# Kernel optimization log

Measured on AMD Instinct MI355X. Metric: run time of the kernel, lower is better.

Reference implementation:

```python
import jax, jax.numpy as jnp
import numpy as np

NUM_SIN = 8
HIDDEN = 64
COND = 128
OUT = 4
SQRT2 = 1.4142135623730951


def coords_to_sinusoidals(coords):
    # coords: [..., 2]; per-frequency blocks of 4: [sin_x, sin_y, cos_x, cos_y]
    freqs = 2.0 ** jnp.arange(NUM_SIN, dtype=coords.dtype)  # mult freq_type, multiplier=2
    ang = coords[..., None, :] * freqs[:, None]              # [..., 8, 2]
    emb = jnp.concatenate([jnp.sin(ang), jnp.cos(ang)], axis=-1)  # [..., 8, 4]
    return emb.reshape(coords.shape[:-1] + (2 * 2 * NUM_SIN,))


def equal_linear(x, w, b, lrelu):
    scale = 1.0 / np.sqrt(w.shape[1])  # lr_mul = 1
    y = x @ (w * scale).T + b
    if lrelu:
        y = jax.nn.leaky_relu(y, 0.2) * SQRT2  # fused_lrelu
    return y


def setup_inputs() -> dict:
    key = jax.random.key(0)
    ks = jax.random.split(key, 8)
    coords = jax.random.normal(ks[0], (8, 256, 256, 2), dtype=jnp.float32)
    c = jax.random.normal(ks[1], (8, COND), dtype=jnp.float32)
    freq_unlock = jax.random.uniform(ks[2], (1,), dtype=jnp.float32)
    in1 = 2 * 2 * NUM_SIN + COND  # 160
    in2 = HIDDEN + COND           # 192
    w1 = jax.random.normal(ks[3], (HIDDEN, in1), dtype=jnp.float32)
    w2 = jax.random.normal(ks[4], (HIDDEN, in2), dtype=jnp.float32)
    w3 = jax.random.normal(ks[5], (HIDDEN, in2), dtype=jnp.float32)
    w4 = jax.random.normal(ks[6], (OUT, in2), dtype=jnp.float32)
    b1 = jnp.zeros((HIDDEN,), jnp.float32)
    b2 = jnp.zeros((HIDDEN,), jnp.float32)
    b3 = jnp.zeros((HIDDEN,), jnp.float32)
    b4 = jnp.zeros((OUT,), jnp.float32)
    return {"coords": coords, "c": c, "freq_unlock": freq_unlock,
            "w1": w1, "b1": b1, "w2": w2, "b2": b2,
            "w3": w3, "b3": b3, "w4": w4, "b4": b4}


def reference(coords, c, freq_unlock, w1, b1, w2, b2, w3, b3, w4, b4):
    B, H, W, _ = coords.shape
    emb = coords_to_sinusoidals(coords / 10.0)  # [B,H,W,32]
    # progressive frequency masking
    limits = jnp.arange(1, NUM_SIN + 1, dtype=coords.dtype) / (NUM_SIN + 1)
    weights = jnp.clip((freq_unlock[0] - limits) * (NUM_SIN + 1), 0.0, 1.0)  # [8]
    emb = emb * jnp.repeat(weights, 4)  # blocks of 4 per frequency
    x = emb.reshape(B * H * W, -1)
    cf = jnp.broadcast_to(c[:, None, None, :], (B, H, W, COND)).reshape(B * H * W, COND)
    h = equal_linear(jnp.concatenate([x, cf], -1), w1, b1, True)
    h = equal_linear(jnp.concatenate([h, cf], -1), w2, b2, True)
    h = equal_linear(jnp.concatenate([h, cf], -1), w3, b3, True)
    h = equal_linear(jnp.concatenate([h, cf], -1), w4, b4, False)
    out = h.reshape(B, H, W, OUT)
    # radius masking
    radius = jnp.sqrt(jnp.sum(coords ** 2, axis=-1, keepdims=True))
    out = out * (1.0 - jnp.tanh(jax.nn.relu(radius - 1.0)))
    return out
```

## Files before the change

kernel.cpp:

```cpp
#include <hip/hip_runtime.h>
#include <math.h>


typedef _Float16 half2v __attribute__((ext_vector_type(2)));
typedef __fp16   fp16x2 __attribute__((ext_vector_type(2)));
typedef _Float16 half4v __attribute__((ext_vector_type(4)));
typedef _Float16 half8  __attribute__((ext_vector_type(8)));
typedef float f32x16 __attribute__((ext_vector_type(16)));

#define SCALE1 0.0790569415042094833f
#define SCALE2 0.0721687836487032206f
#define SQRT2F 1.41421356237309515f

#define FE_L1 0
#define FE_L2 256
#define FE_L3 768
#define FE_L4 1280
#define FE_TOT 1536
#define OFF_CB1 6144
#define OFF_CB2 6656
#define OFF_CB3 7168
#define OFF_CB4 7680

__global__ __launch_bounds__(256) void prep_kernel(
    const float* __restrict__ c, const float* __restrict__ fu,
    const float* __restrict__ w1, const float* __restrict__ b1,
    const float* __restrict__ w2, const float* __restrict__ b2,
    const float* __restrict__ w3, const float* __restrict__ b3,
    const float* __restrict__ w4, const float* __restrict__ b4,
    float* __restrict__ ws)
{
  int t = blockIdx.x * 256 + threadIdx.x;
  if (t < 12288) {
    _Float16* fr = (_Float16*)ws;
    int e, Ktm;
    const float* w; float scale; int stride; bool perm;
    if (t < 2048)       { e = t;         Ktm = 2; w = w1; scale = SCALE1;          stride = 160; perm = false; }
    else if (t < 6144)  { e = t - 2048;  Ktm = 4; w = w2; scale = SCALE2 * SQRT2F; stride = 192; perm = true;  }
    else if (t < 10240) { e = t - 6144;  Ktm = 4; w = w3; scale = SCALE2 * SQRT2F; stride = 192; perm = true;  }
    else                { e = t - 10240; Ktm = 4; w = w4; scale = SCALE2 * SQRT2F; stride = 192; perm = true;  }
    int til  = e >> 9;
    int lane = (e >> 3) & 63;
    int r    = e & 7;
    int q    = lane >> 5;
    int mt = til / Ktm, kt = til - mt * Ktm;
    int j = 32 * mt + (lane & 31);
    int k;
    if (perm) {
      k = 32 * (kt >> 1) + 16 * (kt & 1) + 8 * (r >> 2) + 4 * q + (r & 3);
    } else {
      k = 16 * kt + 8 * q + r;
    }
    float val;
    if (t < 2048) {
      float mw = (fu[0] - (float)((k >> 2) + 1) * (1.0f / 9.0f)) * 9.0f;
      mw = fminf(fmaxf(mw, 0.0f), 1.0f);
      val = w[j * stride + k] * scale * mw;
    } else if (t >= 10240) {
      val = (j < 4) ? w[j * stride + k] * scale : 0.0f;
    } else {
      val = w[j * stride + k] * scale;
    }
    fr[t] = (_Float16)val;
  } else if (t < 12288 + 2048) {
    int u = t - 12288;
    int grp = u >> 9;
    const float* wr; float bias; float scale; int outoff;
    int b, j;
    if (grp < 3) {
      b = (u & 511) >> 6; j = u & 63;
      if (grp == 0)      { wr = w1 + j * 160 + 32; bias = b1[j]; scale = SCALE1; outoff = OFF_CB1 + b * 64 + j; }
      else if (grp == 1) { wr = w2 + j * 192 + 64; bias = b2[j]; scale = SCALE2; outoff = OFF_CB2 + b * 64 + j; }
      else               { wr = w3 + j * 192 + 64; bias = b3[j]; scale = SCALE2; outoff = OFF_CB3 + b * 64 + j; }
    } else {
      int u2 = u - 1536;
      if (u2 >= 32) return;
      b = u2 >> 2; j = u2 & 3;
      wr = w4 + j * 192 + 64; bias = b4[j]; scale = SCALE2; outoff = OFF_CB4 + b * 4 + j;
    }
    const float4* wv = (const float4*)wr;
    const float4* cv = (const float4*)(c + b * 128);
    float4 s = make_float4(0.f, 0.f, 0.f, 0.f);
    #pragma unroll
    for (int k = 0; k < 32; ++k) {
      float4 a = wv[k], d = cv[k];
      s.x = fmaf(a.x, d.x, s.x);
      s.y = fmaf(a.y, d.y, s.y);
      s.z = fmaf(a.z, d.z, s.z);
      s.w = fmaf(a.w, d.w, s.w);
    }
    float dot = (s.x + s.y) + (s.z + s.w);
    ws[outoff] = fmaf(scale, dot, bias);
  }
}

__global__ __launch_bounds__(256, 4) void decoder_main(
    const float2* __restrict__ coords, const float* __restrict__ ws,
    float4* __restrict__ out)
{
  __shared__ __align__(16) _Float16 sfr_raw[FE_TOT * 8];
  __shared__ __align__(16) float scb[256];
  half8* __restrict__ sfr = (half8*)sfr_raw;

  const int tid  = threadIdx.x;
  const int lane = tid & 63;
  const int wave = tid >> 6;
  const int b    = blockIdx.x >> 7;
  const int col  = lane & 31;
  const bool hi  = lane >= 32;
  const int q4   = hi ? 4 : 0;

  const half8* __restrict__ gfr = (const half8*)ws;
  #pragma unroll
  for (int i = 0; i < 6; ++i) {
    const int e0 = wave * 64 + 256 * i;
    __builtin_amdgcn_global_load_lds(
        (const __attribute__((address_space(1))) void*)(gfr + e0 + lane),
        (__attribute__((address_space(3))) void*)(sfr_raw + e0 * 8),
        16, 0, 0);
  }
  if (wave == 3) {
    __builtin_amdgcn_global_load_lds(
        (const __attribute__((address_space(1))) void*)(ws + OFF_CB1 + b * 64 + lane),
        (__attribute__((address_space(3))) void*)(scb + 0), 4, 0, 0);
    __builtin_amdgcn_global_load_lds(
        (const __attribute__((address_space(1))) void*)(ws + OFF_CB2 + b * 64 + lane),
        (__attribute__((address_space(3))) void*)(scb + 64), 4, 0, 0);
    __builtin_amdgcn_global_load_lds(
        (const __attribute__((address_space(1))) void*)(ws + OFF_CB3 + b * 64 + lane),
        (__attribute__((address_space(3))) void*)(scb + 128), 4, 0, 0);
    __builtin_amdgcn_global_load_lds(
        (const __attribute__((address_space(1))) void*)(ws + OFF_CB4 + b * 4 + lane),
        (__attribute__((address_space(3))) void*)(scb + 192), 4, 0, 0);
  }

  const float2* __restrict__ cptr = coords + blockIdx.x * 512 + wave * 64;
  float2 cc[2][2];
  cc[0][0] = cptr[col];       cc[0][1] = cptr[32 + col];
  cc[1][0] = cptr[256 + col]; cc[1][1] = cptr[288 + col];

  f32x16 acc[2][2];
  half8 nbf[2][4];

  auto transition = [&]() {
    #pragma unroll
    for (int mt = 0; mt < 2; ++mt)
      #pragma unroll
      for (int nt = 0; nt < 2; ++nt) {
        #pragma unroll
        for (int h = 0; h < 2; ++h) {
          half2v pp[4];
          #pragma unroll
          for (int p = 0; p < 4; ++p) {
            fp16x2 t = __builtin_amdgcn_cvt_pkrtz(acc[mt][nt][8 * h + 2 * p],
                                                  acc[mt][nt][8 * h + 2 * p + 1]);
            pp[p] = __builtin_bit_cast(half2v, t);
          }
          half4v q0 = __builtin_shufflevector(pp[0], pp[1], 0, 1, 2, 3);
          half4v q1 = __builtin_shufflevector(pp[2], pp[3], 0, 1, 2, 3);
          half8 f = __builtin_shufflevector(q0, q1, 0, 1, 2, 3, 4, 5, 6, 7);
          half8 f2 = f * (_Float16)0.2f;
          nbf[nt][2 * mt + h] = __builtin_elementwise_max(f, f2);
        }
      }
  };

  auto init_acc = [&](const float* __restrict__ cb) {
    #pragma unroll
    for (int mt = 0; mt < 2; ++mt)
      #pragma unroll
      for (int g = 0; g < 4; ++g) {
        const float4 f = *(const float4*)(cb + 32 * mt + 8 * g + q4);
        #pragma unroll
        for (int nt = 0; nt < 2; ++nt) {
          acc[mt][nt][4 * g + 0] = f.x;
          acc[mt][nt][4 * g + 1] = f.y;
          acc[mt][nt][4 * g + 2] = f.z;
          acc[mt][nt][4 * g + 3] = f.w;
        }
      }
  };

  #pragma unroll
  for (int t = 0; t < 2; ++t) {
    half8 bf[2][2];
    {
      const float qm = hi ? 0.4f : 0.1f;
      auto chain = [](float a, float* s, float* c) {
        float s0 = __sinf(a), c0 = __cosf(a);
        s[0] = s0; c[0] = c0;
        float s1 = 2.f * s0 * c0, c1 = (c0 - s0) * (c0 + s0);
        s[1] = s1; c[1] = c1;
        float s2 = 2.f * s1 * c1, c2 = (c1 - s1) * (c1 + s1);
        float s3 = 2.f * s2 * c2, c3 = (c2 - s2) * (c2 + s2);
        float s4 = 2.f * s3 * c3, c4 = (c3 - s3) * (c3 + s3);
        s[2] = s4; c[2] = c4;
        float s5 = 2.f * s4 * c4, c5 = (c4 - s4) * (c4 + s4);
        s[3] = s5; c[3] = c5;
      };
      #pragma unroll
      for (int nt = 0; nt < 2; ++nt) {
        const float2 ccv = cc[t][nt];
        float sx[4], cx[4], sy[4], cy[4];
        chain(ccv.x * qm, sx, cx);
        chain(ccv.y * qm, sy, cy);
        #pragma unroll
        for (int kt = 0; kt < 2; ++kt) {
          const int i0 = 2 * kt, i1 = 2 * kt + 1;
          half2v p0v = __builtin_bit_cast(half2v, __builtin_amdgcn_cvt_pkrtz(sx[i0], sy[i0]));
          half2v p1v = __builtin_bit_cast(half2v, __builtin_amdgcn_cvt_pkrtz(cx[i0], cy[i0]));
          half2v p2v = __builtin_bit_cast(half2v, __builtin_amdgcn_cvt_pkrtz(sx[i1], sy[i1]));
          half2v p3v = __builtin_bit_cast(half2v, __builtin_amdgcn_cvt_pkrtz(cx[i1], cy[i1]));
          half4v q0 = __builtin_shufflevector(p0v, p1v, 0, 1, 2, 3);
          half4v q1 = __builtin_shufflevector(p2v, p3v, 0, 1, 2, 3);
          bf[nt][kt] = __builtin_shufflevector(q0, q1, 0, 1, 2, 3, 4, 5, 6, 7);
        }
      }
    }

    if (t == 0) __syncthreads();

    init_acc(scb + 0);
    #pragma unroll
    for (int kt = 0; kt < 2; ++kt) {
      half8 a0 = sfr[FE_L1 + (0 * 2 + kt) * 64 + lane];
      half8 a1 = sfr[FE_L1 + (1 * 2 + kt) * 64 + lane];
      acc[0][0] = __builtin_amdgcn_mfma_f32_32x32x16_f16(a0, bf[0][kt], acc[0][0], 0, 0, 0);
      acc[0][1] = __builtin_amdgcn_mfma_f32_32x32x16_f16(a0, bf[1][kt], acc[0][1], 0, 0, 0);
      acc[1][0] = __builtin_amdgcn_mfma_f32_32x32x16_f16(a1, bf[0][kt], acc[1][0], 0, 0, 0);
      acc[1][1] = __builtin_amdgcn_mfma_f32_32x32x16_f16(a1, bf[1][kt], acc[1][1], 0, 0, 0);
    }
    transition();

    #pragma unroll
    for (int layer = 0; layer < 2; ++layer) {
      const int fe = layer == 0 ? FE_L2 : FE_L3;
      init_acc(layer == 0 ? scb + 64 : scb + 128);
      #pragma unroll
      for (int kt = 0; kt < 4; ++kt) {
        half8 a0 = sfr[fe + (0 * 4 + kt) * 64 + lane];
        half8 a1 = sfr[fe + (1 * 4 + kt) * 64 + lane];
        acc[0][0] = __builtin_amdgcn_mfma_f32_32x32x16_f16(a0, nbf[0][kt], acc[0][0], 0, 0, 0);
        acc[0][1] = __builtin_amdgcn_mfma_f32_32x32x16_f16(a0, nbf[1][kt], acc[0][1], 0, 0, 0);
        acc[1][0] = __builtin_amdgcn_mfma_f32_32x32x16_f16(a1, nbf[0][kt], acc[1][0], 0, 0, 0);
        acc[1][1] = __builtin_amdgcn_mfma_f32_32x32x16_f16(a1, nbf[1][kt], acc[1][1], 0, 0, 0);
      }
      transition();
    }

    f32x16 acc4[2];
    {
      const float c0 = scb[192], c1 = scb[193], c2 = scb[194], c3 = scb[195];
      #pragma unroll
      for (int r = 0; r < 16; ++r) { acc4[0][r] = 0.f; acc4[1][r] = 0.f; }
      if (!hi) {
        acc4[0][0] = c0; acc4[0][1] = c1; acc4[0][2] = c2; acc4[0][3] = c3;
        acc4[1][0] = c0; acc4[1][1] = c1; acc4[1][2] = c2; acc4[1][3] = c3;
      }
    }
    #pragma unroll
    for (int kt = 0; kt < 4; ++kt) {
      half8 a0 = sfr[FE_L4 + kt * 64 + lane];
      acc4[0] = __builtin_amdgcn_mfma_f32_32x32x16_f16(a0, nbf[0][kt], acc4[0], 0, 0, 0);
      acc4[1] = __builtin_amdgcn_mfma_f32_32x32x16_f16(a0, nbf[1][kt], acc4[1], 0, 0, 0);
    }

    if (!hi) {
      const int pbase = blockIdx.x * 512 + t * 256 + wave * 64 + col;
      #pragma unroll
      for (int nt = 0; nt < 2; ++nt) {
        const float2 ccv = cc[t][nt];
        const float rad = sqrtf(ccv.x * ccv.x + ccv.y * ccv.y);
        const float tt = fmaxf(rad - 1.0f, 0.0f);
        const float m = 2.0f / (__expf(2.0f * tt) + 1.0f);
        out[pbase + 32 * nt] = make_float4(acc4[nt][0] * m, acc4[nt][1] * m,
                                           acc4[nt][2] * m, acc4[nt][3] * m);
      }
    }
  }
}

extern "C" void kernel_launch(void* const* d_in, const int* in_sizes, int n_in,
                              void* d_out, int out_size, void* d_ws, size_t ws_size,
                              hipStream_t stream) {
  const float* coords = (const float*)d_in[0];
  const float* c      = (const float*)d_in[1];
  const float* fu     = (const float*)d_in[2];
  const float* w1     = (const float*)d_in[3];
  const float* b1     = (const float*)d_in[4];
  const float* w2     = (const float*)d_in[5];
  const float* b2     = (const float*)d_in[6];
  const float* w3     = (const float*)d_in[7];
  const float* b3     = (const float*)d_in[8];
  const float* w4     = (const float*)d_in[9];
  const float* b4     = (const float*)d_in[10];
  float* ws  = (float*)d_ws;
  float* out = (float*)d_out;

  int npix = in_sizes[0] / 2;

  prep_kernel<<<56, 256, 0, stream>>>(c, fu, w1, b1, w2, b2, w3, b3, w4, b4, ws);
  decoder_main<<<npix / 512, 256, 0, stream>>>(
      (const float2*)coords, ws, (float4*)out);
}
```

Before: 95.67 us.

## Split weight staging waits per layer and parallelize prep dot products

The decoder kernel now issues coordinate loads first, then bias and weight LDS loads in two halves. It replaces the single __syncthreads with partial vmcnt waits plus s_barrier, so layers 1-2 can start while layer 3-4 weights are still arriving. The prep kernel splits each 128-wide conditioning dot product across four lanes with shuffle reductions and launches more blocks to shorten its critical path. The hand-written waitcnt counts rely on the compiler's load ordering, which the sched_barrier calls are meant to preserve.

```diff
diff --git a/kernel.cpp b/kernel.cpp
--- a/kernel.cpp
+++ b/kernel.cpp
@@ -62,37 +62,43 @@
       val = w[j * stride + k] * scale;
     }
     fr[t] = (_Float16)val;
-  } else if (t < 12288 + 2048) {
+  } else {
     int u = t - 12288;
-    int grp = u >> 9;
+    if (u >= 6272) return;
+    int d = u >> 2, part = u & 3;
     const float* wr; float bias; float scale; int outoff;
     int b, j;
-    if (grp < 3) {
-      b = (u & 511) >> 6; j = u & 63;
+    if (d < 1536) {
+      int grp = d >> 9;
+      b = (d & 511) >> 6; j = d & 63;
       if (grp == 0)      { wr = w1 + j * 160 + 32; bias = b1[j]; scale = SCALE1; outoff = OFF_CB1 + b * 64 + j; }
       else if (grp == 1) { wr = w2 + j * 192 + 64; bias = b2[j]; scale = SCALE2; outoff = OFF_CB2 + b * 64 + j; }
       else               { wr = w3 + j * 192 + 64; bias = b3[j]; scale = SCALE2; outoff = OFF_CB3 + b * 64 + j; }
     } else {
-      int u2 = u - 1536;
-      if (u2 >= 32) return;
+      int u2 = d - 1536;
       b = u2 >> 2; j = u2 & 3;
       wr = w4 + j * 192 + 64; bias = b4[j]; scale = SCALE2; outoff = OFF_CB4 + b * 4 + j;
     }
-    const float4* wv = (const float4*)wr;
-    const float4* cv = (const float4*)(c + b * 128);
+    const float4* wv = (const float4*)wr + part * 8;
+    const float4* cv = (const float4*)(c + b * 128) + part * 8;
     float4 s = make_float4(0.f, 0.f, 0.f, 0.f);
     #pragma unroll
-    for (int k = 0; k < 32; ++k) {
-      float4 a = wv[k], d = cv[k];
-      s.x = fmaf(a.x, d.x, s.x);
-      s.y = fmaf(a.y, d.y, s.y);
-      s.z = fmaf(a.z, d.z, s.z);
-      s.w = fmaf(a.w, d.w, s.w);
-    }
-    float dot = (s.x + s.y) + (s.z + s.w);
-    ws[outoff] = fmaf(scale, dot, bias);
+    for (int k = 0; k < 8; ++k) {
+      float4 a = wv[k], dd = cv[k];
+      s.x = fmaf(a.x, dd.x, s.x);
+      s.y = fmaf(a.y, dd.y, s.y);
+      s.z = fmaf(a.z, dd.z, s.z);
+      s.w = fmaf(a.w, dd.w, s.w);
+    }
+    float v = (s.x + s.y) + (s.z + s.w);
+    v += __shfl_xor(v, 1);
+    v += __shfl_xor(v, 2);
+    if (part == 0) ws[outoff] = fmaf(scale, v, bias);
   }
 }
+
+#define WAIT_VM3() asm volatile("s_waitcnt vmcnt(3)" ::: "memory")
+#define WAIT_VM0() asm volatile("s_waitcnt vmcnt(0)" ::: "memory")
 
 __global__ __launch_bounds__(256, 4) void decoder_main(
     const float2* __restrict__ coords, const float* __restrict__ ws,
@@ -110,34 +116,47 @@
   const bool hi  = lane >= 32;
   const int q4   = hi ? 4 : 0;
 
-  const half8* __restrict__ gfr = (const half8*)ws;
-  #pragma unroll
-  for (int i = 0; i < 6; ++i) {
-    const int e0 = wave * 64 + 256 * i;
-    __builtin_amdgcn_global_load_lds(
-        (const __attribute__((address_space(1))) void*)(gfr + e0 + lane),
-        (__attribute__((address_space(3))) void*)(sfr_raw + e0 * 8),
-        16, 0, 0);
-  }
-  if (wave == 3) {
-    __builtin_amdgcn_global_load_lds(
-        (const __attribute__((address_space(1))) void*)(ws + OFF_CB1 + b * 64 + lane),
-        (__attribute__((address_space(3))) void*)(scb + 0), 4, 0, 0);
-    __builtin_amdgcn_global_load_lds(
-        (const __attribute__((address_space(1))) void*)(ws + OFF_CB2 + b * 64 + lane),
-        (__attribute__((address_space(3))) void*)(scb + 64), 4, 0, 0);
-    __builtin_amdgcn_global_load_lds(
-        (const __attribute__((address_space(1))) void*)(ws + OFF_CB3 + b * 64 + lane),
-        (__attribute__((address_space(3))) void*)(scb + 128), 4, 0, 0);
-    __builtin_amdgcn_global_load_lds(
-        (const __attribute__((address_space(1))) void*)(ws + OFF_CB4 + b * 4 + lane),
-        (__attribute__((address_space(3))) void*)(scb + 192), 4, 0, 0);
-  }
-
   const float2* __restrict__ cptr = coords + blockIdx.x * 512 + wave * 64;
   float2 cc[2][2];
   cc[0][0] = cptr[col];       cc[0][1] = cptr[32 + col];
   cc[1][0] = cptr[256 + col]; cc[1][1] = cptr[288 + col];
+  __builtin_amdgcn_sched_barrier(0);
+
+  if (wave == 3) {
+    __builtin_amdgcn_global_load_lds(
+        (const __attribute__((address_space(1))) void*)(ws + OFF_CB1 + b * 64 + lane),
+        (__attribute__((address_space(3))) void*)(scb + 0), 4, 0, 0);
+    __builtin_amdgcn_global_load_lds(
+        (const __attribute__((address_space(1))) void*)(ws + OFF_CB2 + b * 64 + lane),
+        (__attribute__((address_space(3))) void*)(scb + 64), 4, 0, 0);
+    __builtin_amdgcn_global_load_lds(
+        (const __attribute__((address_space(1))) void*)(ws + OFF_CB3 + b * 64 + lane),
+        (__attribute__((address_space(3))) void*)(scb + 128), 4, 0, 0);
+    __builtin_amdgcn_global_load_lds(
+        (const __attribute__((address_space(1))) void*)(ws + OFF_CB4 + b * 4 + lane),
+        (__attribute__((address_space(3))) void*)(scb + 192), 4, 0, 0);
+  }
+  __builtin_amdgcn_sched_barrier(0);
+
+  const half8* __restrict__ gfr = (const half8*)ws;
+  #pragma unroll
+  for (int i = 0; i < 3; ++i) {
+    const int e0 = wave * 64 + 256 * i;
+    __builtin_amdgcn_global_load_lds(
+        (const __attribute__((address_space(1))) void*)(gfr + e0 + lane),
+        (__attribute__((address_space(3))) void*)(sfr_raw + e0 * 8),
+        16, 0, 0);
+  }
+  __builtin_amdgcn_sched_barrier(0);
+  #pragma unroll
+  for (int i = 3; i < 6; ++i) {
+    const int e0 = wave * 64 + 256 * i;
+    __builtin_amdgcn_global_load_lds(
+        (const __attribute__((address_space(1))) void*)(gfr + e0 + lane),
+        (__attribute__((address_space(3))) void*)(sfr_raw + e0 * 8),
+        16, 0, 0);
+  }
+  __builtin_amdgcn_sched_barrier(0);
 
   f32x16 acc[2][2];
   half8 nbf[2][4];
@@ -218,7 +237,11 @@
       }
     }
 
-    if (t == 0) __syncthreads();
+    if (t == 0) {
+      WAIT_VM3();
+      __builtin_amdgcn_s_barrier();
+      __builtin_amdgcn_sched_barrier(0);
+    }
 
     init_acc(scb + 0);
     #pragma unroll
@@ -232,21 +255,35 @@
     }
     transition();
 
-    #pragma unroll
-    for (int layer = 0; layer < 2; ++layer) {
-      const int fe = layer == 0 ? FE_L2 : FE_L3;
-      init_acc(layer == 0 ? scb + 64 : scb + 128);
-      #pragma unroll
-      for (int kt = 0; kt < 4; ++kt) {
-        half8 a0 = sfr[fe + (0 * 4 + kt) * 64 + lane];
-        half8 a1 = sfr[fe + (1 * 4 + kt) * 64 + lane];
-        acc[0][0] = __builtin_amdgcn_mfma_f32_32x32x16_f16(a0, nbf[0][kt], acc[0][0], 0, 0, 0);
-        acc[0][1] = __builtin_amdgcn_mfma_f32_32x32x16_f16(a0, nbf[1][kt], acc[0][1], 0, 0, 0);
-        acc[1][0] = __builtin_amdgcn_mfma_f32_32x32x16_f16(a1, nbf[0][kt], acc[1][0], 0, 0, 0);
-        acc[1][1] = __builtin_amdgcn_mfma_f32_32x32x16_f16(a1, nbf[1][kt], acc[1][1], 0, 0, 0);
-      }
-      transition();
-    }
+    init_acc(scb + 64);
+    #pragma unroll
+    for (int kt = 0; kt < 4; ++kt) {
+      half8 a0 = sfr[FE_L2 + (0 * 4 + kt) * 64 + lane];
+      half8 a1 = sfr[FE_L2 + (1 * 4 + kt) * 64 + lane];
+      acc[0][0] = __builtin_amdgcn_mfma_f32_32x32x16_f16(a0, nbf[0][kt], acc[0][0], 0, 0, 0);
+      acc[0][1] = __builtin_amdgcn_mfma_f32_32x32x16_f16(a0, nbf[1][kt], acc[0][1], 0, 0, 0);
+      acc[1][0] = __builtin_amdgcn_mfma_f32_32x32x16_f16(a1, nbf[0][kt], acc[1][0], 0, 0, 0);
+      acc[1][1] = __builtin_amdgcn_mfma_f32_32x32x16_f16(a1, nbf[1][kt], acc[1][1], 0, 0, 0);
+    }
+    transition();
+
+    if (t == 0) {
+      WAIT_VM0();
+      __builtin_amdgcn_s_barrier();
+      __builtin_amdgcn_sched_barrier(0);
+    }
+
+    init_acc(scb + 128);
+    #pragma unroll
+    for (int kt = 0; kt < 4; ++kt) {
+      half8 a0 = sfr[FE_L3 + (0 * 4 + kt) * 64 + lane];
+      half8 a1 = sfr[FE_L3 + (1 * 4 + kt) * 64 + lane];
+      acc[0][0] = __builtin_amdgcn_mfma_f32_32x32x16_f16(a0, nbf[0][kt], acc[0][0], 0, 0, 0);
+      acc[0][1] = __builtin_amdgcn_mfma_f32_32x32x16_f16(a0, nbf[1][kt], acc[0][1], 0, 0, 0);
+      acc[1][0] = __builtin_amdgcn_mfma_f32_32x32x16_f16(a1, nbf[0][kt], acc[1][0], 0, 0, 0);
+      acc[1][1] = __builtin_amdgcn_mfma_f32_32x32x16_f16(a1, nbf[1][kt], acc[1][1], 0, 0, 0);
+    }
+    transition();
 
     f32x16 acc4[2];
     {
@@ -299,7 +336,7 @@
 
   int npix = in_sizes[0] / 2;
 
-  prep_kernel<<<56, 256, 0, stream>>>(c, fu, w1, b1, w2, b2, w3, b3, w4, b4, ws);
+  prep_kernel<<<73, 256, 0, stream>>>(c, fu, w1, b1, w2, b2, w3, b3, w4, b4, ws);
   decoder_main<<<npix / 512, 256, 0, stream>>>(
       (const float2*)coords, ws, (float4*)out);
 }
```

Result: faster. 92.70 us (-3.1%).
